# Optimization experiments

Hardware: AMD Instinct MI355X
Metric: run time of the kernel (lower is better)

The kernel has to match this reference:

```python
import jax, jax.numpy as jnp
import numpy as np

EPS = 1e-4

def softmax_kernel(data, projection, is_query):
    # data: [b,h,s,d], projection: [m,d] -> phi(data): [b,h,s,m]
    d = data.shape[-1]
    m = projection.shape[0]
    data_normalizer = d ** -0.25
    ratio = m ** -0.5
    # projected logits
    data_dash = jnp.einsum('bhsd,md->bhsm', data_normalizer * data, projection)
    # ||x||^2 / 2 * normalizer^2, per token
    diag_data = 0.5 * (data_normalizer ** 2) * jnp.sum(data * data, axis=-1, keepdims=True)
    if is_query:
        stab = jnp.max(data_dash, axis=-1, keepdims=True)          # per-token max
    else:
        stab = jnp.max(data_dash, axis=(-2, -1), keepdims=True)    # per (b,h) max
    return ratio * (jnp.exp(data_dash - diag_data - stab) + EPS)

def setup_inputs() -> dict:
    key = jax.random.key(0)
    kq, kk, kp = jax.random.split(key, 3)
    b, h, s, d, m = 2, 16, 4096, 64, 256
    q = jax.random.normal(kq, (b, h, s, d), dtype=jnp.float32)
    k = jax.random.normal(kk, (b, h, s, d), dtype=jnp.float32)
    projection_matrix = jax.random.normal(kp, (m, d), dtype=jnp.float32)
    return {"q": q, "k": k, "projection_matrix": projection_matrix}

def reference(q, k, projection_matrix):
    q_prime = softmax_kernel(q, projection_matrix, is_query=True)
    k_prime = softmax_kernel(k, projection_matrix, is_query=False)
    return (q_prime, k_prime)
```

## Files before the change

### kernel.cpp

```cpp
#include <hip/hip_runtime.h>
#include <math.h>

#define D 64
#define M 256
#define QOUT_ELEMS 33554432ull

constexpr float DATA_NORM = 0.35355339059327373f;
constexpr float L2E       = 1.4426950408889634f;
constexpr float DN_L2E    = DATA_NORM * L2E;
constexpr float DIAG_L2E  = 0.0625f * L2E;
constexpr float RATIO     = 0.0625f;
constexpr float EPS_F     = 1e-4f;

__global__ __launch_bounds__(256) void k0_transpose(const float* __restrict__ proj,
                                                    float* __restrict__ projT) {
    int i = blockIdx.x * 256 + threadIdx.x;
    int m = i >> 6, d = i & 63;
    projT[d * M + m] = proj[i];
}

__global__ __launch_bounds__(512, 4) void k1_main(
    const float* __restrict__ qin, const float* __restrict__ kin,
    const float* __restrict__ projT, float* __restrict__ out,
    float* __restrict__ partial_max)
{
    __shared__ float proj_lds[D * M];
    __shared__ float x_lds[8][8][D];

    const int tid  = threadIdx.x;
    const int lane = tid & 63;
    const int wave = tid >> 6;
    const int bid  = blockIdx.x;
    const bool is_q = (bid < 512);
    const float* __restrict__ src = is_q ? qin : kin;
    const int tb = is_q ? bid : (bid - 512);
    float* __restrict__ outbase = out + (is_q ? 0ull : QOUT_ELEMS);

    {
        const float4* g = (const float4*)projT;
        float4* l = (float4*)proj_lds;
        #pragma unroll
        for (int i = 0; i < 8; ++i) l[i * 512 + tid] = g[i * 512 + tid];
    }
    __syncthreads();

    float blockmax = -INFINITY;

    for (int pass = 0; pass < 4; ++pass) {
        const int token0 = tb * 256 + pass * 64 + wave * 8;

        const float4* g = (const float4*)(src + (size_t)token0 * D);
        float4* xl = (float4*)(&x_lds[wave][0][0]);
        float4 xv[2];
        #pragma unroll
        for (int kk = 0; kk < 2; ++kk) xv[kk] = g[kk * 64 + lane];
        #pragma unroll
        for (int kk = 0; kk < 2; ++kk) xl[kk * 64 + lane] = xv[kk];

        float dsum[2];
        #pragma unroll
        for (int kk = 0; kk < 2; ++kk)
            dsum[kk] = xv[kk].x*xv[kk].x + xv[kk].y*xv[kk].y
                     + xv[kk].z*xv[kk].z + xv[kk].w*xv[kk].w;
        #pragma unroll
        for (int off = 1; off < 16; off <<= 1) {
            #pragma unroll
            for (int kk = 0; kk < 2; ++kk)
                dsum[kk] += __shfl_xor(dsum[kk], off);
        }
        float diag[8];
        #pragma unroll
        for (int tt = 0; tt < 8; ++tt)
            diag[tt] = __shfl(dsum[tt >> 2], (tt & 3) * 16) * DIAG_L2E;

        __syncthreads();

        float4 acc[8];
        #pragma unroll
        for (int tt = 0; tt < 8; ++tt) acc[tt] = make_float4(0.f, 0.f, 0.f, 0.f);

        for (int d4 = 0; d4 < 16; ++d4) {
            float4 pv[4];
            #pragma unroll
            for (int i = 0; i < 4; ++i)
                pv[i] = *(const float4*)&proj_lds[(4 * d4 + i) * M + 4 * lane];
            #pragma unroll
            for (int tt = 0; tt < 8; ++tt) {
                float4 xq = *(const float4*)&x_lds[wave][tt][4 * d4];
                acc[tt].x = fmaf(pv[0].x, xq.x, acc[tt].x);
                acc[tt].y = fmaf(pv[0].y, xq.x, acc[tt].y);
                acc[tt].z = fmaf(pv[0].z, xq.x, acc[tt].z);
                acc[tt].w = fmaf(pv[0].w, xq.x, acc[tt].w);
                acc[tt].x = fmaf(pv[1].x, xq.y, acc[tt].x);
                acc[tt].y = fmaf(pv[1].y, xq.y, acc[tt].y);
                acc[tt].z = fmaf(pv[1].z, xq.y, acc[tt].z);
                acc[tt].w = fmaf(pv[1].w, xq.y, acc[tt].w);
                acc[tt].x = fmaf(pv[2].x, xq.z, acc[tt].x);
                acc[tt].y = fmaf(pv[2].y, xq.z, acc[tt].y);
                acc[tt].z = fmaf(pv[2].z, xq.z, acc[tt].z);
                acc[tt].w = fmaf(pv[2].w, xq.z, acc[tt].w);
                acc[tt].x = fmaf(pv[3].x, xq.w, acc[tt].x);
                acc[tt].y = fmaf(pv[3].y, xq.w, acc[tt].y);
                acc[tt].z = fmaf(pv[3].z, xq.w, acc[tt].z);
                acc[tt].w = fmaf(pv[3].w, xq.w, acc[tt].w);
            }
        }

        if (is_q) {
            #pragma unroll
            for (int tt = 0; tt < 8; ++tt) {
                float4 dd;
                dd.x = acc[tt].x * DN_L2E;
                dd.y = acc[tt].y * DN_L2E;
                dd.z = acc[tt].z * DN_L2E;
                dd.w = acc[tt].w * DN_L2E;
                float mx = fmaxf(fmaxf(dd.x, dd.y), fmaxf(dd.z, dd.w));
                #pragma unroll
                for (int off = 1; off < 64; off <<= 1)
                    mx = fmaxf(mx, __shfl_xor(mx, off));
                const float c = diag[tt] + mx;
                float4 o;
                o.x = RATIO * (exp2f(dd.x - c) + EPS_F);
                o.y = RATIO * (exp2f(dd.y - c) + EPS_F);
                o.z = RATIO * (exp2f(dd.z - c) + EPS_F);
                o.w = RATIO * (exp2f(dd.w - c) + EPS_F);
                ((float4*)outbase)[(size_t)(token0 + tt) * 64 + lane] = o;
            }
        } else {
            #pragma unroll
            for (int tt = 0; tt < 8; ++tt) {
                float4 dd;
                dd.x = acc[tt].x * DN_L2E;
                dd.y = acc[tt].y * DN_L2E;
                dd.z = acc[tt].z * DN_L2E;
                dd.w = acc[tt].w * DN_L2E;
                blockmax = fmaxf(blockmax, fmaxf(fmaxf(dd.x, dd.y), fmaxf(dd.z, dd.w)));
                float4 o;
                o.x = dd.x - diag[tt];
                o.y = dd.y - diag[tt];
                o.z = dd.z - diag[tt];
                o.w = dd.w - diag[tt];
                ((float4*)outbase)[(size_t)(token0 + tt) * 64 + lane] = o;
            }
        }
        __syncthreads();
    }

    if (!is_q) {
        #pragma unroll
        for (int off = 1; off < 64; off <<= 1)
            blockmax = fmaxf(blockmax, __shfl_xor(blockmax, off));
        if (lane == 0) x_lds[0][0][wave] = blockmax;
        __syncthreads();
        if (tid == 0) {
            float m0 = -INFINITY;
            #pragma unroll
            for (int w = 0; w < 8; ++w) m0 = fmaxf(m0, x_lds[0][0][w]);
            partial_max[tb] = m0;
        }
    }
}

__global__ __launch_bounds__(256) void k3_fix(float* __restrict__ outk,
                                              const float* __restrict__ partial) {
    const int bid = blockIdx.x;
    const int bh  = bid >> 6;
    const int tid = threadIdx.x;
    float v = partial[bh * 16 + (tid & 15)];
    #pragma unroll
    for (int off = 1; off < 16; off <<= 1)
        v = fmaxf(v, __shfl_xor(v, off));
    const float st = v;

    float4* p = (float4*)outk + (size_t)bid * 4096;
    #pragma unroll 4
    for (int it = 0; it < 16; ++it) {
        float4 w = p[it * 256 + tid];
        float4 o;
        o.x = RATIO * (exp2f(w.x - st) + EPS_F);
        o.y = RATIO * (exp2f(w.y - st) + EPS_F);
        o.z = RATIO * (exp2f(w.z - st) + EPS_F);
        o.w = RATIO * (exp2f(w.w - st) + EPS_F);
        p[it * 256 + tid] = o;
    }
}

extern "C" void kernel_launch(void* const* d_in, const int* in_sizes, int n_in,
                              void* d_out, int out_size, void* d_ws, size_t ws_size,
                              hipStream_t stream) {
    const float* q    = (const float*)d_in[0];
    const float* k    = (const float*)d_in[1];
    const float* proj = (const float*)d_in[2];
    float* out = (float*)d_out;
    float* ws  = (float*)d_ws;

    float* projT   = ws;
    float* partial = ws + 16384;

    k0_transpose<<<64,   256, 0, stream>>>(proj, projT);
    k1_main     <<<1024, 512, 0, stream>>>(q, k, projT, out, partial);
    k3_fix      <<<2048, 256, 0, stream>>>(out + QOUT_ELEMS, partial);
}
```

Measured before the change: 423.9 us.

## Hold projection slice in registers instead of LDS and split columns across wave pairs

Each lane now keeps its two projection columns for all 64 dims in registers (128 floats), which drops the 64KB LDS projection tile and the per-iteration LDS loads of it. Waves are paired: each group of 16 tokens is handled by two waves that each compute half of the 256 outputs, so the query row max needs a cross-wave reduction through LDS and an extra barrier. Launch bounds drop to 2 blocks per SM to allow the large register footprint. The risks are register pressure and spills, lower occupancy, and narrower float2 stores.

```diff
diff --git a/kernel.cpp b/kernel.cpp
--- a/kernel.cpp
+++ b/kernel.cpp
@@ -19,128 +19,117 @@
     projT[d * M + m] = proj[i];
 }
 
-__global__ __launch_bounds__(512, 4) void k1_main(
+__global__ __launch_bounds__(512, 2) void k1_main(
     const float* __restrict__ qin, const float* __restrict__ kin,
     const float* __restrict__ projT, float* __restrict__ out,
     float* __restrict__ partial_max)
 {
-    __shared__ float proj_lds[D * M];
-    __shared__ float x_lds[8][8][D];
+    __shared__ float x_lds[4][16][D];
+    __shared__ float diag_lds[4][16];
+    __shared__ float hm_lds[4][2][16];
+    __shared__ float wmax_lds[8];
 
     const int tid  = threadIdx.x;
     const int lane = tid & 63;
     const int wave = tid >> 6;
+    const int grp  = wave & 3;
+    const int half = wave >> 2;
     const int bid  = blockIdx.x;
     const bool is_q = (bid < 512);
     const float* __restrict__ src = is_q ? qin : kin;
     const int tb = is_q ? bid : (bid - 512);
     float* __restrict__ outbase = out + (is_q ? 0ull : QOUT_ELEMS);
 
+    float2 pr[D];
     {
-        const float4* g = (const float4*)projT;
-        float4* l = (float4*)proj_lds;
+        const float* pbase = projT + half * 128 + 2 * lane;
         #pragma unroll
-        for (int i = 0; i < 8; ++i) l[i * 512 + tid] = g[i * 512 + tid];
+        for (int d = 0; d < D; ++d)
+            pr[d] = *(const float2*)(pbase + d * M);
     }
-    __syncthreads();
 
     float blockmax = -INFINITY;
 
     for (int pass = 0; pass < 4; ++pass) {
-        const int token0 = tb * 256 + pass * 64 + wave * 8;
+        const int token0 = tb * 256 + pass * 64 + grp * 16;
 
-        const float4* g = (const float4*)(src + (size_t)token0 * D);
-        float4* xl = (float4*)(&x_lds[wave][0][0]);
-        float4 xv[2];
-        #pragma unroll
-        for (int kk = 0; kk < 2; ++kk) xv[kk] = g[kk * 64 + lane];
-        #pragma unroll
-        for (int kk = 0; kk < 2; ++kk) xl[kk * 64 + lane] = xv[kk];
-
-        float dsum[2];
-        #pragma unroll
-        for (int kk = 0; kk < 2; ++kk)
-            dsum[kk] = xv[kk].x*xv[kk].x + xv[kk].y*xv[kk].y
-                     + xv[kk].z*xv[kk].z + xv[kk].w*xv[kk].w;
-        #pragma unroll
-        for (int off = 1; off < 16; off <<= 1) {
+        if (half == 0) {
+            const float4* g = (const float4*)(src + (size_t)token0 * D);
+            float4* xl = (float4*)(&x_lds[grp][0][0]);
+            float4 xv[4];
             #pragma unroll
-            for (int kk = 0; kk < 2; ++kk)
-                dsum[kk] += __shfl_xor(dsum[kk], off);
+            for (int kk = 0; kk < 4; ++kk) xv[kk] = g[kk * 64 + lane];
+            #pragma unroll
+            for (int kk = 0; kk < 4; ++kk) xl[kk * 64 + lane] = xv[kk];
+            float ds_[4];
+            #pragma unroll
+            for (int kk = 0; kk < 4; ++kk)
+                ds_[kk] = xv[kk].x*xv[kk].x + xv[kk].y*xv[kk].y
+                        + xv[kk].z*xv[kk].z + xv[kk].w*xv[kk].w;
+            #pragma unroll
+            for (int off = 1; off < 16; off <<= 1) {
+                #pragma unroll
+                for (int kk = 0; kk < 4; ++kk)
+                    ds_[kk] += __shfl_xor(ds_[kk], off);
+            }
+            if ((lane & 15) == 0) {
+                #pragma unroll
+                for (int kk = 0; kk < 4; ++kk)
+                    diag_lds[grp][kk * 4 + (lane >> 4)] = ds_[kk] * DIAG_L2E;
+            }
         }
-        float diag[8];
-        #pragma unroll
-        for (int tt = 0; tt < 8; ++tt)
-            diag[tt] = __shfl(dsum[tt >> 2], (tt & 3) * 16) * DIAG_L2E;
-
         __syncthreads();
 
-        float4 acc[8];
+        float2 acc[16];
         #pragma unroll
-        for (int tt = 0; tt < 8; ++tt) acc[tt] = make_float4(0.f, 0.f, 0.f, 0.f);
+        for (int tt = 0; tt < 16; ++tt) acc[tt] = make_float2(0.f, 0.f);
 
+        #pragma unroll
         for (int d4 = 0; d4 < 16; ++d4) {
-            float4 pv[4];
             #pragma unroll
-            for (int i = 0; i < 4; ++i)
-                pv[i] = *(const float4*)&proj_lds[(4 * d4 + i) * M + 4 * lane];
-            #pragma unroll
-            for (int tt = 0; tt < 8; ++tt) {
-                float4 xq = *(const float4*)&x_lds[wave][tt][4 * d4];
-                acc[tt].x = fmaf(pv[0].x, xq.x, acc[tt].x);
-                acc[tt].y = fmaf(pv[0].y, xq.x, acc[tt].y);
-                acc[tt].z = fmaf(pv[0].z, xq.x, acc[tt].z);
-                acc[tt].w = fmaf(pv[0].w, xq.x, acc[tt].w);
-                acc[tt].x = fmaf(pv[1].x, xq.y, acc[tt].x);
-                acc[tt].y = fmaf(pv[1].y, xq.y, acc[tt].y);
-                acc[tt].z = fmaf(pv[1].z, xq.y, acc[tt].z);
-                acc[tt].w = fmaf(pv[1].w, xq.y, acc[tt].w);
-                acc[tt].x = fmaf(pv[2].x, xq.z, acc[tt].x);
-                acc[tt].y = fmaf(pv[2].y, xq.z, acc[tt].y);
-                acc[tt].z = fmaf(pv[2].z, xq.z, acc[tt].z);
-                acc[tt].w = fmaf(pv[2].w, xq.z, acc[tt].w);
-                acc[tt].x = fmaf(pv[3].x, xq.w, acc[tt].x);
-                acc[tt].y = fmaf(pv[3].y, xq.w, acc[tt].y);
-                acc[tt].z = fmaf(pv[3].z, xq.w, acc[tt].z);
-                acc[tt].w = fmaf(pv[3].w, xq.w, acc[tt].w);
+            for (int tt = 0; tt < 16; ++tt) {
+                float4 xq = *(const float4*)&x_lds[grp][tt][4 * d4];
+                acc[tt].x = fmaf(pr[4*d4+0].x, xq.x, acc[tt].x);
+                acc[tt].y = fmaf(pr[4*d4+0].y, xq.x, acc[tt].y);
+                acc[tt].x = fmaf(pr[4*d4+1].x, xq.y, acc[tt].x);
+                acc[tt].y = fmaf(pr[4*d4+1].y, xq.y, acc[tt].y);
+                acc[tt].x = fmaf(pr[4*d4+2].x, xq.z, acc[tt].x);
+                acc[tt].y = fmaf(pr[4*d4+2].y, xq.z, acc[tt].y);
+                acc[tt].x = fmaf(pr[4*d4+3].x, xq.w, acc[tt].x);
+                acc[tt].y = fmaf(pr[4*d4+3].y, xq.w, acc[tt].y);
             }
         }
 
         if (is_q) {
             #pragma unroll
-            for (int tt = 0; tt < 8; ++tt) {
-                float4 dd;
-                dd.x = acc[tt].x * DN_L2E;
-                dd.y = acc[tt].y * DN_L2E;
-                dd.z = acc[tt].z * DN_L2E;
-                dd.w = acc[tt].w * DN_L2E;
-                float mx = fmaxf(fmaxf(dd.x, dd.y), fmaxf(dd.z, dd.w));
+            for (int tt = 0; tt < 16; ++tt) {
+                float hx = fmaxf(acc[tt].x, acc[tt].y) * DN_L2E;
                 #pragma unroll
                 for (int off = 1; off < 64; off <<= 1)
-                    mx = fmaxf(mx, __shfl_xor(mx, off));
-                const float c = diag[tt] + mx;
-                float4 o;
-                o.x = RATIO * (exp2f(dd.x - c) + EPS_F);
-                o.y = RATIO * (exp2f(dd.y - c) + EPS_F);
-                o.z = RATIO * (exp2f(dd.z - c) + EPS_F);
-                o.w = RATIO * (exp2f(dd.w - c) + EPS_F);
-                ((float4*)outbase)[(size_t)(token0 + tt) * 64 + lane] = o;
+                    hx = fmaxf(hx, __shfl_xor(hx, off));
+                if (lane == 0) hm_lds[grp][half][tt] = hx;
+            }
+            __syncthreads();
+            float2* ob2 = (float2*)outbase;
+            #pragma unroll
+            for (int tt = 0; tt < 16; ++tt) {
+                const float stab = fmaxf(hm_lds[grp][0][tt], hm_lds[grp][1][tt]);
+                const float c = diag_lds[grp][tt] + stab;
+                float2 o;
+                o.x = RATIO * (exp2f(acc[tt].x * DN_L2E - c) + EPS_F);
+                o.y = RATIO * (exp2f(acc[tt].y * DN_L2E - c) + EPS_F);
+                ob2[(size_t)(token0 + tt) * 128 + half * 64 + lane] = o;
             }
         } else {
+            float2* ob2 = (float2*)outbase;
             #pragma unroll
-            for (int tt = 0; tt < 8; ++tt) {
-                float4 dd;
-                dd.x = acc[tt].x * DN_L2E;
-                dd.y = acc[tt].y * DN_L2E;
-                dd.z = acc[tt].z * DN_L2E;
-                dd.w = acc[tt].w * DN_L2E;
-                blockmax = fmaxf(blockmax, fmaxf(fmaxf(dd.x, dd.y), fmaxf(dd.z, dd.w)));
-                float4 o;
-                o.x = dd.x - diag[tt];
-                o.y = dd.y - diag[tt];
-                o.z = dd.z - diag[tt];
-                o.w = dd.w - diag[tt];
-                ((float4*)outbase)[(size_t)(token0 + tt) * 64 + lane] = o;
+            for (int tt = 0; tt < 16; ++tt) {
+                const float ddx = acc[tt].x * DN_L2E;
+                const float ddy = acc[tt].y * DN_L2E;
+                blockmax = fmaxf(blockmax, fmaxf(ddx, ddy));
+                const float dg = diag_lds[grp][tt];
+                ob2[(size_t)(token0 + tt) * 128 + half * 64 + lane] =
+                    make_float2(ddx - dg, ddy - dg);
             }
         }
         __syncthreads();
@@ -150,12 +139,12 @@
         #pragma unroll
         for (int off = 1; off < 64; off <<= 1)
             blockmax = fmaxf(blockmax, __shfl_xor(blockmax, off));
-        if (lane == 0) x_lds[0][0][wave] = blockmax;
+        if (lane == 0) wmax_lds[wave] = blockmax;
         __syncthreads();
         if (tid == 0) {
             float m0 = -INFINITY;
             #pragma unroll
-            for (int w = 0; w < 8; ++w) m0 = fmaxf(m0, x_lds[0][0][w]);
+            for (int w = 0; w < 8; ++w) m0 = fmaxf(m0, wmax_lds[w]);
             partial_max[tb] = m0;
         }
     }
```

Result: slower. 556.8 us (+31.3%).
